# Kernel tuning notes

Hardware: AMD Instinct MI355X
Metric: run time of the kernel (lower is better)

Reference implementation:

```python
import jax, jax.numpy as jnp
import numpy as np

NUM_ENT = 500000
NUM_REL = 500
EMBED = 128
HIDDEN = 256
N_NODES = 8192          # 2 * batch_size (pairs flattened)
N_EDGES = 524288        # total ragged neighbors


def setup_inputs() -> dict:
    key = jax.random.key(0)
    ks = jax.random.split(key, 12)
    entities = jax.random.randint(ks[0], (N_NODES,), 0, NUM_ENT, dtype=jnp.int64 if jax.config.jax_enable_x64 else jnp.int32)
    neighbor_entities = jax.random.randint(ks[1], (N_EDGES,), 0, NUM_ENT)
    neighbor_relations = jax.random.randint(ks[2], (N_EDGES,), 0, NUM_REL)
    offsets = jnp.sort(jax.random.randint(ks[3], (N_NODES,), 0, N_EDGES))
    offsets = offsets.at[0].set(0)  # embedding_bag requires offsets[0] == 0
    entity_emb = jax.random.normal(ks[4], (NUM_ENT, EMBED), dtype=jnp.float32) * 0.02
    relation_emb = jax.random.normal(ks[5], (NUM_REL, EMBED), dtype=jnp.float32) * 0.02
    W_t = jax.random.normal(ks[6], (HIDDEN, EMBED), dtype=jnp.float32) * (1.0 / np.sqrt(EMBED))
    b_t = jnp.zeros((HIDDEN,), jnp.float32)
    W_n = jax.random.normal(ks[7], (HIDDEN, 2 * EMBED), dtype=jnp.float32) * (1.0 / np.sqrt(2 * EMBED))
    b_n = jnp.zeros((HIDDEN,), jnp.float32)
    W_r = jax.random.normal(ks[8], (HIDDEN, 2 * HIDDEN), dtype=jnp.float32) * (1.0 / np.sqrt(2 * HIDDEN))
    b_r = jnp.zeros((HIDDEN,), jnp.float32)
    return {
        "entities": entities,
        "neighbor_entities": neighbor_entities,
        "neighbor_relations": neighbor_relations,
        "offsets": offsets,
        "entity_emb": entity_emb,
        "relation_emb": relation_emb,
        "W_t": W_t, "b_t": b_t,
        "W_n": W_n, "b_n": b_n,
        "W_r": W_r, "b_r": b_r,
    }


def reference(entities, neighbor_entities, neighbor_relations, offsets,
              entity_emb, relation_emb, W_t, b_t, W_n, b_n, W_r, b_r):
    n_nodes = entities.shape[0]
    batch_size = n_nodes // 2
    total = neighbor_entities.shape[0]

    # self-entity path: gather + Linear(E -> H)
    ent_h = entity_emb[entities] @ W_t.T + b_t  # [2B, H]

    # embedding_bag(mode='mean') == ragged segment-mean via offsets
    seg = jnp.searchsorted(offsets, jnp.arange(total), side="right") - 1  # [E_total]
    ne_sum = jax.ops.segment_sum(entity_emb[neighbor_entities], seg, num_segments=n_nodes)
    nr_sum = jax.ops.segment_sum(relation_emb[neighbor_relations], seg, num_segments=n_nodes)
    cnt = jax.ops.segment_sum(jnp.ones((total,), entity_emb.dtype), seg, num_segments=n_nodes)
    denom = jnp.maximum(cnt, 1.0)[:, None]  # empty bags -> zeros (torch semantics)

    neighbor = jnp.concatenate([ne_sum / denom, nr_sum / denom], axis=-1)  # [2B, 2E]
    neigh_h = neighbor @ W_n.T + b_n  # [2B, H]

    node = jax.nn.relu(ent_h + neigh_h).reshape(batch_size, -1)  # [B, 2H]
    pair = jax.nn.relu(node @ W_r.T + b_r)  # [B, H]
    return pair
```

## Files before the change

### kernel.cpp

```cpp
#include <hip/hip_runtime.h>

#define NN 8192
#define NEDGE 524288
#define EMB 128
#define TILE 512

typedef __attribute__((ext_vector_type(8))) short bf16x8;
typedef __attribute__((ext_vector_type(4))) float f32x4;

__device__ __forceinline__ ushort f2bf(float f) {
    union { float f; uint u; } v; v.f = f;
    return (ushort)((v.u + 0x7FFF + ((v.u >> 16) & 1)) >> 16);
}

__global__ __launch_bounds__(256) void k_agg_prep(
    const int* __restrict__ entities,
    const int* __restrict__ nbr_ent,
    const int* __restrict__ nbr_rel,
    const int* __restrict__ offsets,
    const float* __restrict__ ent_emb,
    const float* __restrict__ rel_emb,
    const float* __restrict__ Wt,
    const float* __restrict__ Wn,
    const float* __restrict__ bt,
    const float* __restrict__ bn,
    const float* __restrict__ Wr,
    ushort* __restrict__ Xcat,
    ushort* __restrict__ Wb1,
    float* __restrict__ bias1,
    ushort* __restrict__ Wb2)
{
    const int blk = blockIdx.x;
    if (blk >= NN) {
        const int j = blk - NN;
        const int t = threadIdx.x;
        for (int c = t; c < 384; c += 256) {
            const float v = (c < 128) ? Wt[(size_t)j * 128 + c]
                                      : Wn[(size_t)j * 256 + (c - 128)];
            Wb1[(size_t)j * 384 + c] = f2bf(v);
        }
        for (int c = t; c < 512; c += 256)
            Wb2[(size_t)j * 512 + c] = f2bf(Wr[(size_t)j * 512 + c]);
        if (t == 0) bias1[j] = bt[j] + bn[j];
        return;
    }

    const int node  = blk;
    const int start = offsets[node];
    const int end   = (node + 1 < NN) ? offsets[node + 1] : NEDGE;
    const int cnt   = end - start;

    const int g    = threadIdx.x >> 5;
    const int lane = threadIdx.x & 31;
    const int c    = lane * 4;

    __shared__ int   sie[TILE];
    __shared__ int   sir[TILE];
    __shared__ float se[8][32][4];
    __shared__ float sr[8][32][4];

    float4 ae = make_float4(0.f, 0.f, 0.f, 0.f);
    float4 ar = make_float4(0.f, 0.f, 0.f, 0.f);

    for (int tb = start; tb < end; tb += TILE) {
        const int n = min(end - tb, TILE);
        __syncthreads();
        for (int i = threadIdx.x; i < n; i += 256) {
            sie[i] = nbr_ent[tb + i];
            sir[i] = nbr_rel[tb + i];
        }
        __syncthreads();

        for (int i = g; i < n; i += 64) {
            int   idx[8];
            float msk[8];
            #pragma unroll
            for (int j = 0; j < 8; ++j) {
                const int v = (j == 0) ? 1 : (i + 8 * j < n);
                idx[j] = v ? (i + 8 * j) : i;
                msk[j] = (float)v;
            }
            float4 ve[8], vr[8];
            #pragma unroll
            for (int j = 0; j < 8; ++j)
                ve[j] = *(const float4*)(ent_emb + (size_t)sie[idx[j]] * EMB + c);
            #pragma unroll
            for (int j = 0; j < 8; ++j)
                vr[j] = *(const float4*)(rel_emb + (size_t)sir[idx[j]] * EMB + c);
            #pragma unroll
            for (int j = 0; j < 8; ++j) {
                ae.x = fmaf(msk[j], ve[j].x, ae.x);
                ae.y = fmaf(msk[j], ve[j].y, ae.y);
                ae.z = fmaf(msk[j], ve[j].z, ae.z);
                ae.w = fmaf(msk[j], ve[j].w, ae.w);
                ar.x = fmaf(msk[j], vr[j].x, ar.x);
                ar.y = fmaf(msk[j], vr[j].y, ar.y);
                ar.z = fmaf(msk[j], vr[j].z, ar.z);
                ar.w = fmaf(msk[j], vr[j].w, ar.w);
            }
        }
    }

    se[g][lane][0] = ae.x; se[g][lane][1] = ae.y;
    se[g][lane][2] = ae.z; se[g][lane][3] = ae.w;
    sr[g][lane][0] = ar.x; sr[g][lane][1] = ar.y;
    sr[g][lane][2] = ar.z; sr[g][lane][3] = ar.w;
    __syncthreads();

    ushort* xrow = Xcat + (size_t)node * 384;
    if (threadIdx.x < 32) {
        const int l = threadIdx.x;
        float4 te = make_float4(0.f, 0.f, 0.f, 0.f);
        float4 tr = make_float4(0.f, 0.f, 0.f, 0.f);
        #pragma unroll
        for (int o = 0; o < 8; ++o) {
            te.x += se[o][l][0]; te.y += se[o][l][1];
            te.z += se[o][l][2]; te.w += se[o][l][3];
            tr.x += sr[o][l][0]; tr.y += sr[o][l][1];
            tr.z += sr[o][l][2]; tr.w += sr[o][l][3];
        }
        const float inv = 1.0f / (float)(cnt > 1 ? cnt : 1);
        ushort4 ue, ur;
        ue.x = f2bf(te.x * inv); ue.y = f2bf(te.y * inv);
        ue.z = f2bf(te.z * inv); ue.w = f2bf(te.w * inv);
        ur.x = f2bf(tr.x * inv); ur.y = f2bf(tr.y * inv);
        ur.z = f2bf(tr.z * inv); ur.w = f2bf(tr.w * inv);
        *(ushort4*)(xrow + 128 + l * 4) = ue;
        *(ushort4*)(xrow + 256 + l * 4) = ur;
    } else if (threadIdx.x < 64) {
        const int l  = threadIdx.x - 32;
        const int c2 = l * 4;
        const int ent = entities[node];
        const float4 v = *(const float4*)(ent_emb + (size_t)ent * EMB + c2);
        ushort4 u;
        u.x = f2bf(v.x); u.y = f2bf(v.y); u.z = f2bf(v.z); u.w = f2bf(v.w);
        *(ushort4*)(xrow + c2) = u;
    }
}

__global__ __launch_bounds__(256) void k_gemm1(
    const ushort* __restrict__ A,
    const ushort* __restrict__ B,
    const float* __restrict__ bias,
    ushort* __restrict__ H)
{
    const int wave = threadIdx.x >> 6;
    const int lane = threadIdx.x & 63;
    const int m0 = blockIdx.x * 64 + wave * 16;
    const int n0 = blockIdx.y * 64;
    const int lm = lane & 15;
    const int lk = (lane >> 4) * 8;

    const ushort* Ap  = A + (size_t)(m0 + lm) * 384 + lk;
    const ushort* Bp0 = B + (size_t)(n0 +  0 + lm) * 384 + lk;
    const ushort* Bp1 = B + (size_t)(n0 + 16 + lm) * 384 + lk;
    const ushort* Bp2 = B + (size_t)(n0 + 32 + lm) * 384 + lk;
    const ushort* Bp3 = B + (size_t)(n0 + 48 + lm) * 384 + lk;

    f32x4 acc0 = {0.f, 0.f, 0.f, 0.f};
    f32x4 acc1 = {0.f, 0.f, 0.f, 0.f};
    f32x4 acc2 = {0.f, 0.f, 0.f, 0.f};
    f32x4 acc3 = {0.f, 0.f, 0.f, 0.f};

    #pragma unroll
    for (int kb = 0; kb < 12; ++kb) {
        const bf16x8 a  = *(const bf16x8*)(Ap  + kb * 32);
        const bf16x8 b0 = *(const bf16x8*)(Bp0 + kb * 32);
        const bf16x8 b1 = *(const bf16x8*)(Bp1 + kb * 32);
        const bf16x8 b2 = *(const bf16x8*)(Bp2 + kb * 32);
        const bf16x8 b3 = *(const bf16x8*)(Bp3 + kb * 32);
        acc0 = __builtin_amdgcn_mfma_f32_16x16x32_bf16(a, b0, acc0, 0, 0, 0);
        acc1 = __builtin_amdgcn_mfma_f32_16x16x32_bf16(a, b1, acc1, 0, 0, 0);
        acc2 = __builtin_amdgcn_mfma_f32_16x16x32_bf16(a, b2, acc2, 0, 0, 0);
        acc3 = __builtin_amdgcn_mfma_f32_16x16x32_bf16(a, b3, acc3, 0, 0, 0);
    }

    const int r0 = (lane >> 4) * 4;
    f32x4 accs[4] = {acc0, acc1, acc2, acc3};
    #pragma unroll
    for (int ni = 0; ni < 4; ++ni) {
        const int col = n0 + ni * 16 + lm;
        const float bv = bias[col];
        #pragma unroll
        for (int j = 0; j < 4; ++j) {
            const int row = m0 + r0 + j;
            const float v = fmaxf(accs[ni][j] + bv, 0.f);
            H[(size_t)row * 256 + col] = f2bf(v);
        }
    }
}

__global__ __launch_bounds__(256) void k_gemm2(
    const ushort* __restrict__ A,
    const ushort* __restrict__ B,
    const float* __restrict__ bias,
    float* __restrict__ out)
{
    const int wave = threadIdx.x >> 6;
    const int lane = threadIdx.x & 63;
    const int m0 = blockIdx.x * 64 + wave * 16;
    const int n0 = blockIdx.y * 64;
    const int lm = lane & 15;
    const int lk = (lane >> 4) * 8;

    const ushort* Ap  = A + (size_t)(m0 + lm) * 512 + lk;
    const ushort* Bp0 = B + (size_t)(n0 +  0 + lm) * 512 + lk;
    const ushort* Bp1 = B + (size_t)(n0 + 16 + lm) * 512 + lk;
    const ushort* Bp2 = B + (size_t)(n0 + 32 + lm) * 512 + lk;
    const ushort* Bp3 = B + (size_t)(n0 + 48 + lm) * 512 + lk;

    f32x4 acc0 = {0.f, 0.f, 0.f, 0.f};
    f32x4 acc1 = {0.f, 0.f, 0.f, 0.f};
    f32x4 acc2 = {0.f, 0.f, 0.f, 0.f};
    f32x4 acc3 = {0.f, 0.f, 0.f, 0.f};

    #pragma unroll
    for (int kb = 0; kb < 16; ++kb) {
        const bf16x8 a  = *(const bf16x8*)(Ap  + kb * 32);
        const bf16x8 b0 = *(const bf16x8*)(Bp0 + kb * 32);
        const bf16x8 b1 = *(const bf16x8*)(Bp1 + kb * 32);
        const bf16x8 b2 = *(const bf16x8*)(Bp2 + kb * 32);
        const bf16x8 b3 = *(const bf16x8*)(Bp3 + kb * 32);
        acc0 = __builtin_amdgcn_mfma_f32_16x16x32_bf16(a, b0, acc0, 0, 0, 0);
        acc1 = __builtin_amdgcn_mfma_f32_16x16x32_bf16(a, b1, acc1, 0, 0, 0);
        acc2 = __builtin_amdgcn_mfma_f32_16x16x32_bf16(a, b2, acc2, 0, 0, 0);
        acc3 = __builtin_amdgcn_mfma_f32_16x16x32_bf16(a, b3, acc3, 0, 0, 0);
    }

    const int r0 = (lane >> 4) * 4;
    f32x4 accs[4] = {acc0, acc1, acc2, acc3};
    #pragma unroll
    for (int ni = 0; ni < 4; ++ni) {
        const int col = n0 + ni * 16 + lm;
        const float bv = bias[col];
        #pragma unroll
        for (int j = 0; j < 4; ++j) {
            const int row = m0 + r0 + j;
            out[(size_t)row * 256 + col] = fmaxf(accs[ni][j] + bv, 0.f);
        }
    }
}

extern "C" void kernel_launch(void* const* d_in, const int* in_sizes, int n_in,
                              void* d_out, int out_size, void* d_ws, size_t ws_size,
                              hipStream_t stream) {
    const int*   entities = (const int*)d_in[0];
    const int*   nbr_ent  = (const int*)d_in[1];
    const int*   nbr_rel  = (const int*)d_in[2];
    const int*   offsets  = (const int*)d_in[3];
    const float* ent_emb  = (const float*)d_in[4];
    const float* rel_emb  = (const float*)d_in[5];
    const float* W_t      = (const float*)d_in[6];
    const float* b_t      = (const float*)d_in[7];
    const float* W_n      = (const float*)d_in[8];
    const float* b_n      = (const float*)d_in[9];
    const float* W_r      = (const float*)d_in[10];
    const float* b_r      = (const float*)d_in[11];
    float* out = (float*)d_out;

    char* ws = (char*)d_ws;
    ushort* Xcat  = (ushort*)(ws);
    ushort* H     = (ushort*)(ws + 6291456);
    ushort* Wb1   = (ushort*)(ws + 10485760);
    ushort* Wb2   = (ushort*)(ws + 10682368);
    float*  bias1 = (float*)(ws + 10944512);

    hipLaunchKernelGGL(k_agg_prep, dim3(NN + 256), dim3(256), 0, stream,
                       entities, nbr_ent, nbr_rel, offsets, ent_emb, rel_emb,
                       W_t, W_n, b_t, b_n, W_r, Xcat, Wb1, bias1, Wb2);
    hipLaunchKernelGGL(k_gemm1, dim3(NN / 64, 4), dim3(256), 0, stream,
                       Xcat, Wb1, bias1, H);
    hipLaunchKernelGGL(k_gemm2, dim3(NN / 2 / 64, 4), dim3(256), 0, stream,
                       H, Wb2, b_r, out);
}
```

Measured before the change: 77.55 us.

## Fuse the two MLP GEMMs into one kernel with hidden tile kept in LDS

Merges the first GEMM (node hidden) and the pair GEMM into a single kernel. Each block computes 32 node rows of the hidden layer into shared memory, then reads pairs of rows back as the 512-wide pair input for the second GEMM. This removes the global round-trip of H and one kernel launch. In exchange the grid shrinks to 256 blocks, each wave does more work per block, and every block re-reads the full weight matrices.

```diff
diff --git a/kernel.cpp b/kernel.cpp
--- a/kernel.cpp
+++ b/kernel.cpp
@@ -4,6 +4,7 @@
 #define NEDGE 524288
 #define EMB 128
 #define TILE 512
+#define LDP 260
 
 typedef __attribute__((ext_vector_type(8))) short bf16x8;
 typedef __attribute__((ext_vector_type(4))) float f32x4;
@@ -138,105 +139,84 @@
     }
 }
 
-__global__ __launch_bounds__(256) void k_gemm1(
+__global__ __launch_bounds__(256) void k_mlp(
     const ushort* __restrict__ A,
-    const ushort* __restrict__ B,
-    const float* __restrict__ bias,
-    ushort* __restrict__ H)
+    const ushort* __restrict__ B1,
+    const float* __restrict__ bias1,
+    const ushort* __restrict__ B2,
+    const float* __restrict__ br,
+    float* __restrict__ out)
 {
+    __shared__ ushort h_lds[32][LDP];
+
     const int wave = threadIdx.x >> 6;
     const int lane = threadIdx.x & 63;
-    const int m0 = blockIdx.x * 64 + wave * 16;
-    const int n0 = blockIdx.y * 64;
     const int lm = lane & 15;
     const int lk = (lane >> 4) * 8;
-
-    const ushort* Ap  = A + (size_t)(m0 + lm) * 384 + lk;
-    const ushort* Bp0 = B + (size_t)(n0 +  0 + lm) * 384 + lk;
-    const ushort* Bp1 = B + (size_t)(n0 + 16 + lm) * 384 + lk;
-    const ushort* Bp2 = B + (size_t)(n0 + 32 + lm) * 384 + lk;
-    const ushort* Bp3 = B + (size_t)(n0 + 48 + lm) * 384 + lk;
-
-    f32x4 acc0 = {0.f, 0.f, 0.f, 0.f};
-    f32x4 acc1 = {0.f, 0.f, 0.f, 0.f};
-    f32x4 acc2 = {0.f, 0.f, 0.f, 0.f};
-    f32x4 acc3 = {0.f, 0.f, 0.f, 0.f};
-
-    #pragma unroll
-    for (int kb = 0; kb < 12; ++kb) {
-        const bf16x8 a  = *(const bf16x8*)(Ap  + kb * 32);
-        const bf16x8 b0 = *(const bf16x8*)(Bp0 + kb * 32);
-        const bf16x8 b1 = *(const bf16x8*)(Bp1 + kb * 32);
-        const bf16x8 b2 = *(const bf16x8*)(Bp2 + kb * 32);
-        const bf16x8 b3 = *(const bf16x8*)(Bp3 + kb * 32);
-        acc0 = __builtin_amdgcn_mfma_f32_16x16x32_bf16(a, b0, acc0, 0, 0, 0);
-        acc1 = __builtin_amdgcn_mfma_f32_16x16x32_bf16(a, b1, acc1, 0, 0, 0);
-        acc2 = __builtin_amdgcn_mfma_f32_16x16x32_bf16(a, b2, acc2, 0, 0, 0);
-        acc3 = __builtin_amdgcn_mfma_f32_16x16x32_bf16(a, b3, acc3, 0, 0, 0);
-    }
-
     const int r0 = (lane >> 4) * 4;
-    f32x4 accs[4] = {acc0, acc1, acc2, acc3};
-    #pragma unroll
-    for (int ni = 0; ni < 4; ++ni) {
-        const int col = n0 + ni * 16 + lm;
-        const float bv = bias[col];
-        #pragma unroll
-        for (int j = 0; j < 4; ++j) {
-            const int row = m0 + r0 + j;
-            const float v = fmaxf(accs[ni][j] + bv, 0.f);
-            H[(size_t)row * 256 + col] = f2bf(v);
-        }
-    }
-}
-
-__global__ __launch_bounds__(256) void k_gemm2(
-    const ushort* __restrict__ A,
-    const ushort* __restrict__ B,
-    const float* __restrict__ bias,
-    float* __restrict__ out)
-{
-    const int wave = threadIdx.x >> 6;
-    const int lane = threadIdx.x & 63;
-    const int m0 = blockIdx.x * 64 + wave * 16;
-    const int n0 = blockIdx.y * 64;
-    const int lm = lane & 15;
-    const int lk = (lane >> 4) * 8;
-
-    const ushort* Ap  = A + (size_t)(m0 + lm) * 512 + lk;
-    const ushort* Bp0 = B + (size_t)(n0 +  0 + lm) * 512 + lk;
-    const ushort* Bp1 = B + (size_t)(n0 + 16 + lm) * 512 + lk;
-    const ushort* Bp2 = B + (size_t)(n0 + 32 + lm) * 512 + lk;
-    const ushort* Bp3 = B + (size_t)(n0 + 48 + lm) * 512 + lk;
-
-    f32x4 acc0 = {0.f, 0.f, 0.f, 0.f};
-    f32x4 acc1 = {0.f, 0.f, 0.f, 0.f};
-    f32x4 acc2 = {0.f, 0.f, 0.f, 0.f};
-    f32x4 acc3 = {0.f, 0.f, 0.f, 0.f};
-
-    #pragma unroll
-    for (int kb = 0; kb < 16; ++kb) {
-        const bf16x8 a  = *(const bf16x8*)(Ap  + kb * 32);
-        const bf16x8 b0 = *(const bf16x8*)(Bp0 + kb * 32);
-        const bf16x8 b1 = *(const bf16x8*)(Bp1 + kb * 32);
-        const bf16x8 b2 = *(const bf16x8*)(Bp2 + kb * 32);
-        const bf16x8 b3 = *(const bf16x8*)(Bp3 + kb * 32);
-        acc0 = __builtin_amdgcn_mfma_f32_16x16x32_bf16(a, b0, acc0, 0, 0, 0);
-        acc1 = __builtin_amdgcn_mfma_f32_16x16x32_bf16(a, b1, acc1, 0, 0, 0);
-        acc2 = __builtin_amdgcn_mfma_f32_16x16x32_bf16(a, b2, acc2, 0, 0, 0);
-        acc3 = __builtin_amdgcn_mfma_f32_16x16x32_bf16(a, b3, acc3, 0, 0, 0);
-    }
-
-    const int r0 = (lane >> 4) * 4;
-    f32x4 accs[4] = {acc0, acc1, acc2, acc3};
-    #pragma unroll
-    for (int ni = 0; ni < 4; ++ni) {
-        const int col = n0 + ni * 16 + lm;
-        const float bv = bias[col];
-        #pragma unroll
-        for (int j = 0; j < 4; ++j) {
-            const int row = m0 + r0 + j;
-            out[(size_t)row * 256 + col] = fmaxf(accs[ni][j] + bv, 0.f);
+    const int brow0 = blockIdx.x * 32;
+    const int p0    = blockIdx.x * 16;
+
+    {
+        const int m0 = (wave & 1) * 16;
+        const int n0 = (wave >> 1) * 128;
+        const ushort* Ap = A + (size_t)(brow0 + m0 + lm) * 384 + lk;
+
+        f32x4 acc[8];
+        #pragma unroll
+        for (int ni = 0; ni < 8; ++ni) acc[ni] = (f32x4){0.f, 0.f, 0.f, 0.f};
+
+        #pragma unroll 4
+        for (int kb = 0; kb < 12; ++kb) {
+            const bf16x8 a = *(const bf16x8*)(Ap + kb * 32);
+            #pragma unroll
+            for (int ni = 0; ni < 8; ++ni) {
+                const bf16x8 b = *(const bf16x8*)(B1 + (size_t)(n0 + 16 * ni + lm) * 384 + kb * 32 + lk);
+                acc[ni] = __builtin_amdgcn_mfma_f32_16x16x32_bf16(a, b, acc[ni], 0, 0, 0);
+            }
+        }
+
+        #pragma unroll
+        for (int ni = 0; ni < 8; ++ni) {
+            const int col = n0 + 16 * ni + lm;
+            const float bv = bias1[col];
+            #pragma unroll
+            for (int j = 0; j < 4; ++j) {
+                const float v = fmaxf(acc[ni][j] + bv, 0.f);
+                h_lds[m0 + r0 + j][col] = f2bf(v);
+            }
+        }
+    }
+    __syncthreads();
+
+    {
+        const int n0 = wave * 64;
+
+        f32x4 acc[4];
+        #pragma unroll
+        for (int ni = 0; ni < 4; ++ni) acc[ni] = (f32x4){0.f, 0.f, 0.f, 0.f};
+
+        #pragma unroll 4
+        for (int kb = 0; kb < 16; ++kb) {
+            const int hi   = kb >> 3;
+            const int kcol = (kb & 7) * 32 + lk;
+            const bf16x8 a = *(const bf16x8*)(&h_lds[2 * lm + hi][kcol]);
+            #pragma unroll
+            for (int ni = 0; ni < 4; ++ni) {
+                const bf16x8 b = *(const bf16x8*)(B2 + (size_t)(n0 + 16 * ni + lm) * 512 + kb * 32 + lk);
+                acc[ni] = __builtin_amdgcn_mfma_f32_16x16x32_bf16(a, b, acc[ni], 0, 0, 0);
+            }
+        }
+
+        #pragma unroll
+        for (int ni = 0; ni < 4; ++ni) {
+            const int col = n0 + 16 * ni + lm;
+            const float bv = br[col];
+            #pragma unroll
+            for (int j = 0; j < 4; ++j) {
+                const int p = p0 + r0 + j;
+                out[(size_t)p * 256 + col] = fmaxf(acc[ni][j] + bv, 0.f);
+            }
         }
     }
 }
@@ -260,16 +240,13 @@
 
     char* ws = (char*)d_ws;
     ushort* Xcat  = (ushort*)(ws);
-    ushort* H     = (ushort*)(ws + 6291456);
-    ushort* Wb1   = (ushort*)(ws + 10485760);
-    ushort* Wb2   = (ushort*)(ws + 10682368);
-    float*  bias1 = (float*)(ws + 10944512);
+    ushort* Wb1   = (ushort*)(ws + 6291456);
+    ushort* Wb2   = (ushort*)(ws + 6488064);
+    float*  bias1 = (float*)(ws + 6750208);
 
     hipLaunchKernelGGL(k_agg_prep, dim3(NN + 256), dim3(256), 0, stream,
                        entities, nbr_ent, nbr_rel, offsets, ent_emb, rel_emb,
                        W_t, W_n, b_t, b_n, W_r, Xcat, Wb1, bias1, Wb2);
-    hipLaunchKernelGGL(k_gemm1, dim3(NN / 64, 4), dim3(256), 0, stream,
-                       Xcat, Wb1, bias1, H);
-    hipLaunchKernelGGL(k_gemm2, dim3(NN / 2 / 64, 4), dim3(256), 0, stream,
-                       H, Wb2, b_r, out);
-}
+    hipLaunchKernelGGL(k_mlp, dim3(NN / 32), dim3(256), 0, stream,
+                       Xcat, Wb1, bias1, Wb2, b_r, out);
+}
```

Result: slower. 82.19 us (+6.0%).
